# Performance work log

Hardware: AMD Instinct MI355X
Metric: run time of the kernel (lower is better)

## Reference

```python
import jax, jax.numpy as jnp
import numpy as np

SIGMA_MAX = 25.0

def marginal_prob_std(t):
    # VE-SDE std: sqrt((sigma_max^(2t) - 1) / (2 ln sigma_max))
    log_s = jnp.log(SIGMA_MAX)
    return jnp.sqrt((jnp.exp(2.0 * t * log_s) - 1.0) / (2.0 * log_s))

def setup_inputs() -> dict:
    key = jax.random.key(0)
    k1, k2, k3 = jax.random.split(key, 3)
    B, N, d = 16384, 16384, 1
    x = jax.random.normal(k1, (B, d), dtype=jnp.float32)
    t = jax.random.uniform(k2, (B,), dtype=jnp.float32, minval=1e-3, maxval=1.0)
    train_data = jax.random.normal(k3, (N, d), dtype=jnp.float32)
    return {"x": x, "t": t, "train_data": train_data}

def reference(x, t, train_data):
    # x: [B,1], t: [B], train_data: [N,1]
    sigma = marginal_prob_std(t)                       # [B]
    sigma2 = sigma * sigma                             # [B]
    # pairwise squared distance (d=1): [N, B]
    diff = train_data - x[:, 0][None, :]               # [N,1]-[1,B] -> broadcast fails; do explicit
    diff = train_data[:, 0][:, None] - x[:, 0][None, :]  # [N, B]
    pdf = jnp.exp(-0.5 * (diff * diff) / sigma2[None, :])  # [N, B]
    num = jnp.sum(pdf * train_data, axis=0)            # [N,B]*[N,1] -> [B]
    den = jnp.sum(pdf, axis=0)                         # [B]
    den_safe = jnp.where(den == 0.0, 1.0, den)
    evals = jnp.where(den == 0.0, 0.0, num / den_safe) # nan -> 0 as in torch code
    evals = evals[:, None]                             # [B,1]
    return (evals - x) / sigma2[:, None]
```

## Files before the change

kernel.cpp:

```cpp
#include <hip/hip_runtime.h>
#include <math.h>


typedef float v2f __attribute__((ext_vector_type(2)));

#define BLK   256
#define JB    16
#define PARTS 16
#define CH    4096

#if __has_builtin(__builtin_amdgcn_exp2f)
#define EXP2(x) __builtin_amdgcn_exp2f(x)
#else
#define EXP2(x) exp2f(x)
#endif

__device__ __forceinline__ float sigma2_of(float tj) {
  const float TWO_LOG_S = 6.4377516497364011f;
  return (__expf(TWO_LOG_S * tj) - 1.0f) / TWO_LOG_S;
}

__device__ __forceinline__ float4 load_pad(const float* __restrict__ td,
                                           int gi, int N) {
  if (gi + 3 < N) return *(const float4*)(td + gi);
  float4 v;
  v.x = (gi + 0 < N) ? td[gi + 0] : 1e30f;
  v.y = (gi + 1 < N) ? td[gi + 1] : 1e30f;
  v.z = (gi + 2 < N) ? td[gi + 2] : 1e30f;
  v.w = (gi + 3 < N) ? td[gi + 3] : 1e30f;
  return v;
}

__launch_bounds__(BLK, 4)
__global__ void gmm_fused(const float* __restrict__ x,
                          const float* __restrict__ t,
                          const float* __restrict__ td,
                          float* __restrict__ out,
                          int N, int B) {
  __shared__ float lds[2][CH];
  __shared__ float nbuf[PARTS * JB];
  __shared__ float dbuf[PARTS * JB];

  const int tid  = threadIdx.x;
  const int jl   = tid & (JB - 1);
  const int part = tid >> 4;
  const int j    = blockIdx.x * JB + jl;

  float r = 0.0f, y = 0.0f;
  if (j < B) {
    const float HALF_LOG2E = 0.72134752044448170f;
    float s2 = sigma2_of(t[j]);
    r = __fsqrt_rn(HALF_LOG2E / s2);
    y = x[j] * r;
  }

  const v2f rv  = {r, r};
  const v2f nyv = {-y, -y};

  v2f n0 = {0.f, 0.f}, n1 = {0.f, 0.f}, n2 = {0.f, 0.f}, n3 = {0.f, 0.f};
  v2f d0 = {0.f, 0.f}, d1 = {0.f, 0.f}, d2 = {0.f, 0.f}, d3 = {0.f, 0.f};

#define GROUP(v, nacc, dacc)                                            \
  {                                                                     \
    v2f dd = __builtin_elementwise_fma(v, rv, nyv);                     \
    v2f qq = dd * dd;                                                   \
    v2f pp;                                                             \
    pp.x = EXP2(-qq.x); pp.y = EXP2(-qq.y);                             \
    dacc += pp;                                                         \
    nacc = __builtin_elementwise_fma(pp, v, nacc);                      \
  }

  const int NC = (N + CH - 1) / CH;

  {
    float4 s0 = load_pad(td, (tid          ) * 4, N);
    float4 s1 = load_pad(td, (tid +     BLK) * 4, N);
    float4 s2 = load_pad(td, (tid + 2 * BLK) * 4, N);
    float4 s3 = load_pad(td, (tid + 3 * BLK) * 4, N);
    float4* dst = (float4*)lds[0];
    dst[tid]           = s0;
    dst[tid +     BLK] = s1;
    dst[tid + 2 * BLK] = s2;
    dst[tid + 3 * BLK] = s3;
  }
  __syncthreads();

  for (int c = 0; c < NC; ++c) {
    float4 s0 = {0,0,0,0}, s1 = {0,0,0,0}, s2 = {0,0,0,0}, s3 = {0,0,0,0};
    const bool more = (c + 1 < NC);
    if (more) {
      const int nb = (c + 1) * CH;
      s0 = load_pad(td, nb + (tid          ) * 4, N);
      s1 = load_pad(td, nb + (tid +     BLK) * 4, N);
      s2 = load_pad(td, nb + (tid + 2 * BLK) * 4, N);
      s3 = load_pad(td, nb + (tid + 3 * BLK) * 4, N);
    }

    const float4* l4 = (const float4*)lds[c & 1];
    #pragma unroll 4
    for (int k = 0; k < CH / 64; k += 2) {
      float4 v0 = l4[part + 16 * k];
      float4 v1 = l4[part + 16 * k + 16];
      v2f va = {v0.x, v0.y}, vb = {v0.z, v0.w};
      v2f vc = {v1.x, v1.y}, vd = {v1.z, v1.w};
      GROUP(va, n0, d0)
      GROUP(vb, n1, d1)
      GROUP(vc, n2, d2)
      GROUP(vd, n3, d3)
    }

    if (more) {
      float4* dst = (float4*)lds[(c + 1) & 1];
      dst[tid]           = s0;
      dst[tid +     BLK] = s1;
      dst[tid + 2 * BLK] = s2;
      dst[tid + 3 * BLK] = s3;
      __syncthreads();
    }
  }
#undef GROUP

  v2f numv = (n0 + n1) + (n2 + n3);
  v2f denv = (d0 + d1) + (d2 + d3);
  __syncthreads();
  nbuf[part * JB + jl] = numv.x + numv.y;
  dbuf[part * JB + jl] = denv.x + denv.y;
  __syncthreads();

  if (tid < JB && (blockIdx.x * JB + tid) < B) {
    const int jj = blockIdx.x * JB + tid;
    float num = 0.f, den = 0.f;
    #pragma unroll
    for (int p = 0; p < PARTS; ++p) {
      num += nbuf[p * JB + tid];
      den += dbuf[p * JB + tid];
    }
    float sigma2 = sigma2_of(t[jj]);
    float evals = (den == 0.0f) ? 0.0f : (num / den);
    out[jj] = (evals - x[jj]) / sigma2;
  }
}

extern "C" void kernel_launch(void* const* d_in, const int* in_sizes, int n_in,
                              void* d_out, int out_size, void* d_ws, size_t ws_size,
                              hipStream_t stream) {
  const float* x  = (const float*)d_in[0];
  const float* t  = (const float*)d_in[1];
  const float* td = (const float*)d_in[2];
  float* out = (float*)d_out;
  (void)d_ws; (void)ws_size;

  const int B = in_sizes[0];
  const int N = in_sizes[2];

  const int GX = (B + JB - 1) / JB;
  gmm_fused<<<GX, BLK, 0, stream>>>(x, t, td, out, N, B);
}
```

Baseline: 91.95 us.

## Register-block two query points per thread to halve LDS reads per exp

Each thread now handles two query columns (8 lanes × 2 instead of 16 lanes × 1) and 32 partitions of the training data. Every training value loaded from LDS is used for two Gaussian evaluations, halving LDS traffic per exp. The kernel is likely bound by the transcendental exp rate, so the reduced LDS load may matter little. In exchange it raises register pressure and doubles the partial-sum buffer.

```diff
diff --git a/kernel.cpp b/kernel.cpp
--- a/kernel.cpp
+++ b/kernel.cpp
@@ -4,10 +4,11 @@
 
 typedef float v2f __attribute__((ext_vector_type(2)));
 
-#define BLK   256
-#define JB    16
-#define PARTS 16
-#define CH    4096
+#define BLK    256
+#define JB     16
+#define JLANES 8
+#define PARTS  32
+#define CH     4096
 
 #if __has_builtin(__builtin_amdgcn_exp2f)
 #define EXP2(x) __builtin_amdgcn_exp2f(x)
@@ -42,32 +43,45 @@
   __shared__ float dbuf[PARTS * JB];
 
   const int tid  = threadIdx.x;
-  const int jl   = tid & (JB - 1);
-  const int part = tid >> 4;
-  const int j    = blockIdx.x * JB + jl;
+  const int jl   = tid & (JLANES - 1);
+  const int part = tid >> 3;
+  const int j0   = blockIdx.x * JB + jl;
+  const int j1   = j0 + JLANES;
 
-  float r = 0.0f, y = 0.0f;
-  if (j < B) {
-    const float HALF_LOG2E = 0.72134752044448170f;
-    float s2 = sigma2_of(t[j]);
-    r = __fsqrt_rn(HALF_LOG2E / s2);
-    y = x[j] * r;
+  const float HALF_LOG2E = 0.72134752044448170f;
+  float rA = 0.0f, yA = 0.0f, rB = 0.0f, yB = 0.0f;
+  if (j0 < B) {
+    float s2 = sigma2_of(t[j0]);
+    rA = __fsqrt_rn(HALF_LOG2E / s2);
+    yA = x[j0] * rA;
+  }
+  if (j1 < B) {
+    float s2 = sigma2_of(t[j1]);
+    rB = __fsqrt_rn(HALF_LOG2E / s2);
+    yB = x[j1] * rB;
   }
 
-  const v2f rv  = {r, r};
-  const v2f nyv = {-y, -y};
+  const v2f rvA  = {rA, rA};
+  const v2f nyvA = {-yA, -yA};
+  const v2f rvB  = {rB, rB};
+  const v2f nyvB = {-yB, -yB};
 
-  v2f n0 = {0.f, 0.f}, n1 = {0.f, 0.f}, n2 = {0.f, 0.f}, n3 = {0.f, 0.f};
-  v2f d0 = {0.f, 0.f}, d1 = {0.f, 0.f}, d2 = {0.f, 0.f}, d3 = {0.f, 0.f};
+  v2f nA0 = {0.f, 0.f}, nA1 = {0.f, 0.f}, dA0 = {0.f, 0.f}, dA1 = {0.f, 0.f};
+  v2f nB0 = {0.f, 0.f}, nB1 = {0.f, 0.f}, dB0 = {0.f, 0.f}, dB1 = {0.f, 0.f};
 
-#define GROUP(v, nacc, dacc)                                            \
+#define GROUP2(v, nA, dA, nB, dB)                                       \
   {                                                                     \
-    v2f dd = __builtin_elementwise_fma(v, rv, nyv);                     \
-    v2f qq = dd * dd;                                                   \
-    v2f pp;                                                             \
-    pp.x = EXP2(-qq.x); pp.y = EXP2(-qq.y);                             \
-    dacc += pp;                                                         \
-    nacc = __builtin_elementwise_fma(pp, v, nacc);                      \
+    v2f ddA = __builtin_elementwise_fma(v, rvA, nyvA);                  \
+    v2f ddB = __builtin_elementwise_fma(v, rvB, nyvB);                  \
+    v2f qqA = ddA * ddA;                                                \
+    v2f qqB = ddB * ddB;                                                \
+    v2f ppA, ppB;                                                       \
+    ppA.x = EXP2(-qqA.x); ppA.y = EXP2(-qqA.y);                         \
+    ppB.x = EXP2(-qqB.x); ppB.y = EXP2(-qqB.y);                         \
+    dA += ppA;                                                          \
+    dB += ppB;                                                          \
+    nA = __builtin_elementwise_fma(ppA, v, nA);                         \
+    nB = __builtin_elementwise_fma(ppB, v, nB);                         \
   }
 
   const int NC = (N + CH - 1) / CH;
@@ -98,15 +112,15 @@
 
     const float4* l4 = (const float4*)lds[c & 1];
     #pragma unroll 4
-    for (int k = 0; k < CH / 64; k += 2) {
-      float4 v0 = l4[part + 16 * k];
-      float4 v1 = l4[part + 16 * k + 16];
+    for (int k = 0; k < CH / 256; ++k) {
+      float4 v0 = l4[part + 2 * PARTS * k];
+      float4 v1 = l4[part + 2 * PARTS * k + PARTS];
       v2f va = {v0.x, v0.y}, vb = {v0.z, v0.w};
       v2f vc = {v1.x, v1.y}, vd = {v1.z, v1.w};
-      GROUP(va, n0, d0)
-      GROUP(vb, n1, d1)
-      GROUP(vc, n2, d2)
-      GROUP(vd, n3, d3)
+      GROUP2(va, nA0, dA0, nB0, dB0)
+      GROUP2(vb, nA1, dA1, nB1, dB1)
+      GROUP2(vc, nA0, dA0, nB0, dB0)
+      GROUP2(vd, nA1, dA1, nB1, dB1)
     }
 
     if (more) {
@@ -118,13 +132,15 @@
       __syncthreads();
     }
   }
-#undef GROUP
+#undef GROUP2
 
-  v2f numv = (n0 + n1) + (n2 + n3);
-  v2f denv = (d0 + d1) + (d2 + d3);
+  v2f numvA = nA0 + nA1, denvA = dA0 + dA1;
+  v2f numvB = nB0 + nB1, denvB = dB0 + dB1;
   __syncthreads();
-  nbuf[part * JB + jl] = numv.x + numv.y;
-  dbuf[part * JB + jl] = denv.x + denv.y;
+  nbuf[part * JB + jl]          = numvA.x + numvA.y;
+  dbuf[part * JB + jl]          = denvA.x + denvA.y;
+  nbuf[part * JB + jl + JLANES] = numvB.x + numvB.y;
+  dbuf[part * JB + jl + JLANES] = denvB.x + denvB.y;
   __syncthreads();
 
   if (tid < JB && (blockIdx.x * JB + tid) < B) {
```

Measured after the change: 93.55 us. No clear change (+1.7%).
